# Performance work log

Hardware: AMD Instinct MI355X
Metric: run time of the kernel (lower is better)

## Reference

```python
import jax, jax.numpy as jnp
import numpy as np

H = 16  # n_heads


def _ln(x, g, b, eps=1e-5):
    m = x.mean(-1, keepdims=True)
    v = ((x - m) ** 2).mean(-1, keepdims=True)
    return (x - m) / jnp.sqrt(v + eps) * g + b


def setup_inputs() -> dict:
    key = jax.random.key(0)
    ks = jax.random.split(key, 10)
    b, lq, d, dff, L = 2, 1024, 1024, 4096, 4
    s = 0.02
    return {
        "x": jax.random.normal(ks[0], (b, lq, d), jnp.float32),
        "memory_bank": jax.random.normal(ks[1], (L, b, lq, d), jnp.float32),
        "attn_mask": jax.random.bernoulli(ks[2], 0.3, (b, lq, lq)),
        "ln1_g": jnp.ones((d,), jnp.float32),
        "ln1_b": jnp.zeros((d,), jnp.float32),
        "Wq": jax.random.normal(ks[3], (d, d), jnp.float32) * s,
        "Wk": jax.random.normal(ks[4], (d, d), jnp.float32) * s,
        "Wv": jax.random.normal(ks[5], (d, d), jnp.float32) * s,
        "Wo": jax.random.normal(ks[6], (d, d), jnp.float32) * s,
        "ln2_g": jnp.ones((d,), jnp.float32),
        "ln2_b": jnp.zeros((d,), jnp.float32),
        "W1": jax.random.normal(ks[7], (d, dff), jnp.float32) * s,
        "b1": jnp.zeros((dff,), jnp.float32),
        "W2": jax.random.normal(ks[8], (dff, d), jnp.float32) * s,
        "b2": jnp.zeros((d,), jnp.float32),
    }


def reference(x, memory_bank, attn_mask, ln1_g, ln1_b, Wq, Wk, Wv, Wo,
              ln2_g, ln2_b, W1, b1, W2, b2):
    # x: [b, lq, d]; memory_bank: [L, b, lk, d]; attn_mask: [b, lq, lk] bool (True = masked)
    b, lq, d = x.shape
    dh = d // H
    # preprocess_attn: LayerNorm (eval mode -> dropouts are identity)
    q = _ln(x, ln1_g, ln1_b)
    # grow memory bank with current normalized input
    mem = jnp.concatenate([memory_bank, q[None]], axis=0)  # [L+1, b, lk, d]
    L, _, lk, _ = mem.shape
    # projections (bias-free); key/value projected per layer then flattened over (L, lk)
    pq = (q @ Wq).reshape(b, lq, H, dh).transpose(0, 2, 1, 3) * (dh ** -0.5)  # [b,h,lq,dh]
    pk = (mem @ Wk).transpose(1, 0, 2, 3).reshape(b, L * lk, H, dh).transpose(0, 2, 1, 3)
    pv = (mem @ Wv).transpose(1, 0, 2, 3).reshape(b, L * lk, H, dh).transpose(0, 2, 1, 3)
    scores = jnp.einsum('bhqd,bhkd->bhqk', pq, pk)           # [b,h,lq,L*lk]
    scores = scores.reshape(b, H, lq, L, lk)
    scores = jnp.where(attn_mask[:, None, :, None, :], -jnp.inf, scores)
    attn = jax.nn.softmax(scores.reshape(b, H, lq, L * lk), axis=-1)
    ctx = jnp.einsum('bhqk,bhkd->bhqd', attn, pv)            # [b,h,lq,dh]
    ctx = ctx.transpose(0, 2, 1, 3).reshape(b, lq, d)
    attn_out = ctx @ Wo
    # postprocess_attn: residual add
    x2 = x + attn_out
    # FFN: LayerNorm -> Linear -> ReLU -> Linear -> residual
    f = _ln(x2, ln2_g, ln2_b)
    f = jax.nn.relu(f @ W1 + b1) @ W2 + b2
    out = x2 + f
    return (out, mem)
```

## Files before the change

### kernel.cpp

```cpp
#include <hip/hip_runtime.h>
#include <hip/hip_bf16.h>

typedef __attribute__((ext_vector_type(8))) __bf16 bf16x8;
typedef __attribute__((ext_vector_type(4))) __bf16 bf16x4;
typedef __attribute__((ext_vector_type(4))) float f32x4;
typedef __attribute__((ext_vector_type(16))) float f32x16;

#define MFMA16(a, b, c) __builtin_amdgcn_mfma_f32_16x16x32_bf16((a), (b), (c), 0, 0, 0)
#define MFMA32(a, b, c) __builtin_amdgcn_mfma_f32_32x32x16_bf16((a), (b), (c), 0, 0, 0)
#define LOG2E 1.4426950408889634f

static __device__ __forceinline__ float exp2_fast(float x) {
    float r; asm("v_exp_f32 %0, %1" : "=v"(r) : "v"(x)); return r;
}

__device__ __forceinline__ void gll16(const void* g, void* l) {
    __builtin_amdgcn_global_load_lds((const __attribute__((address_space(1))) void*)g,
                                     (__attribute__((address_space(3))) void*)l,
                                     16, 0, 0);
}

__global__ __launch_bounds__(256) void prep_kernel(const float* __restrict__ bank,
                                                   float* __restrict__ mem_out,
                                                   __bf16* __restrict__ membf,
                                                   const float* __restrict__ x,
                                                   const float* __restrict__ g,
                                                   const float* __restrict__ bta,
                                                   float* __restrict__ q_out,
                                                   __bf16* __restrict__ qbf,
                                                   const unsigned char* __restrict__ mask,
                                                   unsigned int* __restrict__ mbits) {
    __shared__ float rs[4], rs2[4];
    int blk = blockIdx.x;
    if (blk < 2048) {
        int i = blk * 256 + threadIdx.x;
        const float4* i4 = (const float4*)bank;
        float4* o4 = (float4*)mem_out;
        for (; i < 2097152; i += 2048 * 256) {
            float4 v = i4[i];
            o4[i] = v;
            if (membf) {
                bf16x4 ob = {(__bf16)v.x, (__bf16)v.y, (__bf16)v.z, (__bf16)v.w};
                ((bf16x4*)membf)[i] = ob;
            }
        }
    } else if (blk < 4096) {
        int row = blk - 2048;
        const float4 v = ((const float4*)(x + (size_t)row * 1024))[threadIdx.x];
        float s = v.x + v.y + v.z + v.w;
        float s2 = v.x * v.x + v.y * v.y + v.z * v.z + v.w * v.w;
#pragma unroll
        for (int off = 1; off < 64; off <<= 1) {
            s += __shfl_xor(s, off);
            s2 += __shfl_xor(s2, off);
        }
        int wv = threadIdx.x >> 6;
        if ((threadIdx.x & 63) == 0) { rs[wv] = s; rs2[wv] = s2; }
        __syncthreads();
        s = rs[0] + rs[1] + rs[2] + rs[3];
        s2 = rs2[0] + rs2[1] + rs2[2] + rs2[3];
        float mean = s * (1.0f / 1024.0f);
        float var = s2 * (1.0f / 1024.0f) - mean * mean;
        float rstd = rsqrtf(var + 1e-5f);
        float4 gg = ((const float4*)g)[threadIdx.x];
        float4 bb = ((const float4*)bta)[threadIdx.x];
        float4 o;
        o.x = (v.x - mean) * rstd * gg.x + bb.x;
        o.y = (v.y - mean) * rstd * gg.y + bb.y;
        o.z = (v.z - mean) * rstd * gg.z + bb.z;
        o.w = (v.w - mean) * rstd * gg.w + bb.w;
        ((float4*)(q_out + (size_t)row * 1024))[threadIdx.x] = o;
        if (qbf) {
            bf16x4 ob = {(__bf16)o.x, (__bf16)o.y, (__bf16)o.z, (__bf16)o.w};
            ((bf16x4*)(qbf + (size_t)row * 1024))[threadIdx.x] = ob;
        }
    } else if (mbits) {
        int row = blk - 4096;
        const unsigned char* mrow = mask + (size_t)row * 1024;
        int w = threadIdx.x >> 6, l = threadIdx.x & 63;
        unsigned long long* dst = (unsigned long long*)(mbits + (size_t)row * 32);
#pragma unroll
        for (int i = 0; i < 4; i++) {
            int key = i * 256 + w * 64 + l;
            unsigned long long bal = __ballot(mrow[key] != 0);
            if (l == 0) dst[i * 4 + w] = bal;
        }
    }
}

__global__ __launch_bounds__(256) void ln_kernel(const float* __restrict__ x,
                                                 const float* __restrict__ g,
                                                 const float* __restrict__ bta,
                                                 __bf16* __restrict__ outb) {
    int row = blockIdx.x;
    const float4 v = ((const float4*)(x + (size_t)row * 1024))[threadIdx.x];
    float s = v.x + v.y + v.z + v.w;
    float s2 = v.x * v.x + v.y * v.y + v.z * v.z + v.w * v.w;
#pragma unroll
    for (int off = 1; off < 64; off <<= 1) {
        s += __shfl_xor(s, off);
        s2 += __shfl_xor(s2, off);
    }
    __shared__ float rs[4], rs2[4];
    int wv = threadIdx.x >> 6;
    if ((threadIdx.x & 63) == 0) { rs[wv] = s; rs2[wv] = s2; }
    __syncthreads();
    s = rs[0] + rs[1] + rs[2] + rs[3];
    s2 = rs2[0] + rs2[1] + rs2[2] + rs2[3];
    float mean = s * (1.0f / 1024.0f);
    float var = s2 * (1.0f / 1024.0f) - mean * mean;
    float rstd = rsqrtf(var + 1e-5f);
    float4 gg = ((const float4*)g)[threadIdx.x];
    float4 bb = ((const float4*)bta)[threadIdx.x];
    bf16x4 ob;
    ob[0] = (__bf16)((v.x - mean) * rstd * gg.x + bb.x);
    ob[1] = (__bf16)((v.y - mean) * rstd * gg.y + bb.y);
    ob[2] = (__bf16)((v.z - mean) * rstd * gg.z + bb.z);
    ob[3] = (__bf16)((v.w - mean) * rstd * gg.w + bb.w);
    ((bf16x4*)(outb + (size_t)row * 1024))[threadIdx.x] = ob;
}

__global__ __launch_bounds__(256) void comb_ln2(const float* __restrict__ pc0,
                                                const float* __restrict__ pc1,
                                                const float* __restrict__ x,
                                                const float* __restrict__ g,
                                                const float* __restrict__ bta,
                                                float* __restrict__ x2,
                                                __bf16* __restrict__ fln) {
    int row = blockIdx.x;
    int idx = row * 256 + threadIdx.x;
    float4 a = ((const float4*)pc0)[idx];
    float4 b = ((const float4*)pc1)[idx];
    float4 r = ((const float4*)x)[idx];
    float4 v;
    v.x = a.x + b.x + r.x;
    v.y = a.y + b.y + r.y;
    v.z = a.z + b.z + r.z;
    v.w = a.w + b.w + r.w;
    ((float4*)x2)[idx] = v;
    float s = v.x + v.y + v.z + v.w;
    float s2 = v.x * v.x + v.y * v.y + v.z * v.z + v.w * v.w;
#pragma unroll
    for (int off = 1; off < 64; off <<= 1) {
        s += __shfl_xor(s, off);
        s2 += __shfl_xor(s2, off);
    }
    __shared__ float rs[4], rs2[4];
    int wv = threadIdx.x >> 6;
    if ((threadIdx.x & 63) == 0) { rs[wv] = s; rs2[wv] = s2; }
    __syncthreads();
    s = rs[0] + rs[1] + rs[2] + rs[3];
    s2 = rs2[0] + rs2[1] + rs2[2] + rs2[3];
    float mean = s * (1.0f / 1024.0f);
    float var = s2 * (1.0f / 1024.0f) - mean * mean;
    float rstd = rsqrtf(var + 1e-5f);
    float4 gg = ((const float4*)g)[threadIdx.x];
    float4 bb = ((const float4*)bta)[threadIdx.x];
    bf16x4 ob;
    ob[0] = (__bf16)((v.x - mean) * rstd * gg.x + bb.x);
    ob[1] = (__bf16)((v.y - mean) * rstd * gg.y + bb.y);
    ob[2] = (__bf16)((v.z - mean) * rstd * gg.z + bb.z);
    ob[3] = (__bf16)((v.w - mean) * rstd * gg.w + bb.w);
    ((bf16x4*)(fln + (size_t)row * 1024))[threadIdx.x] = ob;
}

__device__ __forceinline__ void tr_body(const float* __restrict__ in, __bf16* __restrict__ out,
                                        int K, int N, int k0, int n0) {
    __shared__ float tile[32][33];
    int tx = threadIdx.x & 31, ty = threadIdx.x >> 5;
#pragma unroll
    for (int i = 0; i < 4; i++)
        tile[ty + i * 8][tx] = in[(size_t)(k0 + ty + i * 8) * N + n0 + tx];
    __syncthreads();
#pragma unroll
    for (int i = 0; i < 4; i++)
        out[(size_t)(n0 + ty + i * 8) * K + k0 + tx] = (__bf16)tile[tx][ty + i * 8];
}

__global__ __launch_bounds__(256) void tr_early(const float* __restrict__ Wq,
                                                const float* __restrict__ Wk,
                                                const float* __restrict__ Wv,
                                                __bf16* __restrict__ Wq_t,
                                                __bf16* __restrict__ Wkv_t) {
    int w = blockIdx.x;
    int sel = w >> 10, within = w & 1023;
    const float* in = (sel == 0) ? Wq : ((sel == 1) ? Wk : Wv);
    __bf16* out = (sel == 0) ? Wq_t : (Wkv_t + (size_t)(sel - 1) * 1048576);
    tr_body(in, out, 1024, 1024, (within >> 5) * 32, (within & 31) * 32);
}

__global__ __launch_bounds__(256) void tr_late(const float* __restrict__ Wo,
                                               const float* __restrict__ W1,
                                               const float* __restrict__ W2,
                                               __bf16* __restrict__ Wo_t,
                                               __bf16* __restrict__ W1_t,
                                               __bf16* __restrict__ W2_t) {
    int w = blockIdx.x;
    const float* in;
    __bf16* out;
    int K, N, k0, n0;
    if (w < 1024) {
        in = Wo; out = Wo_t; K = 1024; N = 1024; n0 = (w & 31) * 32; k0 = (w >> 5) * 32;
    } else if (w < 5120) {
        int v = w - 1024;
        in = W1; out = W1_t; K = 1024; N = 4096; n0 = (v & 127) * 32; k0 = (v >> 7) * 32;
    } else {
        int v = w - 5120;
        in = W2; out = W2_t; K = 4096; N = 1024; n0 = (v & 31) * 32; k0 = (v >> 5) * 32;
    }
    tr_body(in, out, K, N, k0, n0);
}

template <int EPI, bool ABF16>
__device__ __forceinline__ void gemm_core(const void* __restrict__ Av,
                                          const __bf16* __restrict__ Bt,
                                          void* __restrict__ Cout,
                                          const float* __restrict__ bias,
                                          const float* __restrict__ res,
                                          int N, int lda, int ldb, int klen,
                                          float scale, int bm, int bn) {
    constexpr int LDA = ABF16 ? 32 : 40;
    __shared__ __bf16 As[128 * LDA];
    __shared__ __bf16 Bs[128 * 32];

    int t = threadIdx.x;
    int lane = t & 63, wave = t >> 6;
    int wm = (wave >> 1) * 64, wn = (wave & 1) * 64;
    int l16 = lane & 15, l4 = lane >> 4;

    f32x4 acc[4][4];
#pragma unroll
    for (int m = 0; m < 4; m++)
#pragma unroll
        for (int n = 0; n < 4; n++) acc[m][n] = (f32x4){0.f, 0.f, 0.f, 0.f};

    int srow = t >> 2;
    int scol = (t & 3) * 8;
    int ar = t >> 1, ak = (t & 1) * 16;
    const __bf16* Ab = (const __bf16*)Av;
    const float* Af = (const float*)Av;

    for (int k0 = 0; k0 < klen; k0 += 32) {
        gll16(Bt + (size_t)(bn + srow) * ldb + (k0 + scol), &Bs[wave * 512]);
        gll16(Bt + (size_t)(bn + 64 + srow) * ldb + (k0 + scol), &Bs[2048 + wave * 512]);
        if constexpr (ABF16) {
            gll16(Ab + (size_t)(bm + srow) * lda + (k0 + scol), &As[wave * 512]);
            gll16(Ab + (size_t)(bm + 64 + srow) * lda + (k0 + scol), &As[2048 + wave * 512]);
        } else {
            const float* ap = Af + (size_t)(bm + ar) * lda + k0 + ak;
            float4 f0 = ((const float4*)ap)[0];
            float4 f1 = ((const float4*)ap)[1];
            float4 f2 = ((const float4*)ap)[2];
            float4 f3 = ((const float4*)ap)[3];
            float ta[16] = {f0.x, f0.y, f0.z, f0.w, f1.x, f1.y, f1.z, f1.w,
                            f2.x, f2.y, f2.z, f2.w, f3.x, f3.y, f3.z, f3.w};
            bf16x8 v0, v1;
#pragma unroll
            for (int j = 0; j < 8; j++) { v0[j] = (__bf16)ta[j]; v1[j] = (__bf16)ta[j + 8]; }
            *(bf16x8*)&As[ar * 40 + ak] = v0;
            *(bf16x8*)&As[ar * 40 + ak + 8] = v1;
        }
        __syncthreads();

        bf16x8 af[4], bfr[4];
#pragma unroll
        for (int m = 0; m < 4; m++) af[m] = *(const bf16x8*)&As[(wm + m * 16 + l16) * LDA + l4 * 8];
#pragma unroll
        for (int n = 0; n < 4; n++) bfr[n] = *(const bf16x8*)&Bs[(wn + n * 16 + l16) * 32 + l4 * 8];
#pragma unroll
        for (int m = 0; m < 4; m++)
#pragma unroll
            for (int n = 0; n < 4; n++) acc[m][n] = MFMA16(af[m], bfr[n], acc[m][n]);
        __syncthreads();
    }

#pragma unroll
    for (int m = 0; m < 4; m++) {
#pragma unroll
        for (int r = 0; r < 4; r++) {
            int row = bm + wm + m * 16 + l4 * 4 + r;
#pragma unroll
            for (int n = 0; n < 4; n++) {
                int col = bn + wn + n * 16 + l16;
                float c = acc[m][n][r];
                size_t idx = (size_t)row * N + col;
                if (EPI == 0) {
                    ((__bf16*)Cout)[idx] = (__bf16)(c * scale);
                } else if (EPI == 1) {
                    ((float*)Cout)[idx] = c + res[idx];
                } else if (EPI == 2) {
                    ((__bf16*)Cout)[idx] = (__bf16)fmaxf(c + bias[col], 0.0f);
                } else if (EPI == 3) {
                    ((float*)Cout)[idx] = c + bias[col] + res[idx];
                } else {
                    ((float*)Cout)[idx] = c;
                }
            }
        }
    }
}

template <int EPI, bool ABF16>
__global__ __launch_bounds__(256) void gemm_bt(const void* __restrict__ Av,
                                               const __bf16* __restrict__ Bt,
                                               void* __restrict__ Cout,
                                               const float* __restrict__ bias,
                                               const float* __restrict__ res,
                                               int N, int K, float scale, int nbx) {
    int q = gridDim.x >> 3;
    int swz = (blockIdx.x & 7) * q + (blockIdx.x >> 3);
    int bn = (swz % nbx) * 128;
    int bm = (swz / nbx) * 128;
    gemm_core<EPI, ABF16>(Av, Bt, Cout, bias, res, N, K, K, K, scale, bm, bn);
}

template <bool ABF16>
__global__ __launch_bounds__(256) void gemm_proj(const void* __restrict__ Akv,
                                                 const __bf16* __restrict__ Wkv_t,
                                                 __bf16* __restrict__ PKV,
                                                 const void* __restrict__ Aq,
                                                 const __bf16* __restrict__ Wq_t,
                                                 __bf16* __restrict__ Pq) {
    int q = gridDim.x >> 3;
    int swz = (blockIdx.x & 7) * q + (blockIdx.x >> 3);
    const void* A;
    const __bf16* B;
    __bf16* C;
    int N, bm, bn;
    float sc;
    if (swz < 1280) {
        A = Akv; B = Wkv_t; C = PKV; N = 2048; sc = 1.0f;
        bn = (swz & 15) * 128; bm = (swz >> 4) * 128;
    } else {
        int p = swz - 1280;
        A = Aq; B = Wq_t; C = Pq; N = 1024; sc = 0.125f * LOG2E;
        bn = (p & 7) * 128; bm = (p >> 3) * 128;
    }
    gemm_core<0, ABF16>(A, B, C, nullptr, nullptr, N, 1024, 1024, 1024, sc, bm, bn);
}

__global__ __launch_bounds__(256) void gemm_w2(const __bf16* __restrict__ h1,
                                               const __bf16* __restrict__ W2_t,
                                               float* __restrict__ pc0,
                                               float* __restrict__ pc1) {
    int q = gridDim.x >> 3;
    int swz = (blockIdx.x & 7) * q + (blockIdx.x >> 3);
    int half = swz >> 7;
    int p = swz & 127;
    int bn = (p & 7) * 128, bm = (p >> 3) * 128;
    int koff = half * 2048;
    gemm_core<4, true>(h1 + koff, W2_t + koff, half ? pc1 : pc0, nullptr, nullptr,
                       1024, 4096, 4096, 2048, 1.0f, bm, bn);
}

__global__ __launch_bounds__(256) void gemm_wo(const __bf16* __restrict__ ctx,
                                               const __bf16* __restrict__ Wo_t,
                                               float* __restrict__ pc0,
                                               float* __restrict__ pc1) {
    int q = gridDim.x >> 3;
    int swz = (blockIdx.x & 7) * q + (blockIdx.x >> 3);
    int half = swz >> 7;
    int p = swz & 127;
    int bn = (p & 7) * 128, bm = (p >> 3) * 128;
    int koff = half * 512;
    gemm_core<4, true>(ctx + koff, Wo_t + koff, half ? pc1 : pc0, nullptr, nullptr,
                       1024, 1024, 1024, 512, 1.0f, bm, bn);
}

__global__ __launch_bounds__(256) void comb_kernel(const float* __restrict__ pc0,
                                                   const float* __restrict__ pc1,
                                                   const float* __restrict__ bias,
                                                   const float* __restrict__ res,
                                                   float* __restrict__ out) {
    int i = blockIdx.x * 256 + threadIdx.x;
    float4 a = ((const float4*)pc0)[i];
    float4 b = ((const float4*)pc1)[i];
    float4 r = ((const float4*)res)[i];
    float4 o;
    o.x = a.x + b.x + r.x;
    o.y = a.y + b.y + r.y;
    o.z = a.z + b.z + r.z;
    o.w = a.w + b.w + r.w;
    if (bias) {
        float4 bb = ((const float4*)bias)[i & 255];
        o.x += bb.x; o.y += bb.y; o.z += bb.z; o.w += bb.w;
    }
    ((float4*)out)[i] = o;
}

__device__ __forceinline__ void softmax_p(const f32x16& s0, const f32x16& s1,
                                          unsigned int mka, unsigned int mkb,
                                          int hi, float& lsum, bf16x8* pf) {
    unsigned int ow[8][2];
#pragma unroll
    for (int g = 0; g < 4; g++) {
        bf16x4 p0, p1;
#pragma unroll
        for (int m = 0; m < 4; m++) {
            float e = exp2_fast(s0[g * 4 + m]);
            e = ((mka >> (g * 8 + hi * 4 + m)) & 1u) ? 0.0f : e;
            lsum += e;
            p0[m] = (__bf16)e;
            float e2 = exp2_fast(s1[g * 4 + m]);
            e2 = ((mkb >> (g * 8 + hi * 4 + m)) & 1u) ? 0.0f : e2;
            lsum += e2;
            p1[m] = (__bf16)e2;
        }
        ow[g][0] = ((unsigned int*)&p0)[0];
        ow[g][1] = ((unsigned int*)&p0)[1];
        ow[4 + g][0] = ((unsigned int*)&p1)[0];
        ow[4 + g][1] = ((unsigned int*)&p1)[1];
    }
#pragma unroll
    for (int ks = 0; ks < 4; ks++) {
        unsigned int a0 = ow[2 * ks][0], b0 = ow[2 * ks + 1][0];
        unsigned int a1 = ow[2 * ks][1], b1 = ow[2 * ks + 1][1];
        asm volatile("v_permlane32_swap_b32 %0, %1" : "+v"(a0), "+v"(b0));
        asm volatile("v_permlane32_swap_b32 %0, %1" : "+v"(a1), "+v"(b1));
        unsigned int* pp = (unsigned int*)&pf[ks];
        pp[0] = a0; pp[1] = a1; pp[2] = b0; pp[3] = b1;
    }
}

#define NCHP 20
__global__ __launch_bounds__(256, 2) void attn_part(const __bf16* __restrict__ Pq,
                                                    const __bf16* __restrict__ PKV,
                                                    const unsigned int* __restrict__ mbits,
                                                    __bf16* __restrict__ pacc,
                                                    float* __restrict__ pl) {
    int bh = blockIdx.x;
    int b = bh >> 4, h = bh & 15;
    int rng = blockIdx.z;
    int wave = threadIdx.x >> 6, lane = threadIdx.x & 63;
    int l32 = lane & 31, hi = lane >> 5;
    int q0 = blockIdx.y * 256 + wave * 64;

    __shared__ __bf16 Ks[2][64][64];
    __shared__ __bf16 Vt[2][64][64];

    bf16x8 qf[2][4];
#pragma unroll
    for (int tile = 0; tile < 2; tile++) {
        const __bf16* pqrow = Pq + (size_t)(b * 1024 + q0 + tile * 32 + l32) * 1024 + h * 64 + hi * 8;
#pragma unroll
        for (int ds = 0; ds < 4; ds++) qf[tile][ds] = *(const bf16x8*)(pqrow + ds * 16);
    }

    f32x16 acc00, acc01, acc10, acc11;
#pragma unroll
    for (int i = 0; i < 16; i++) { acc00[i] = 0.f; acc01[i] = 0.f; acc10[i] = 0.f; acc11[i] = 0.f; }
    float lsum0 = 0.0f, lsum1 = 0.0f;

    const unsigned int* mrow0 = mbits + (size_t)(b * 1024 + q0 + l32) * 32;
    const unsigned int* mrow1 = mbits + (size_t)(b * 1024 + q0 + 32 + l32) * 32;

    int tl = threadIdx.x;
    int skey = tl >> 2, sd0 = (tl & 3) << 4;
    int kgbase = rng * 1280;

    int Gk = (skey ^ (skey >> 3)) & 7;
    int kw0 = skey * 64 + ((((sd0 >> 3) + 0) ^ Gk) << 3);
    int kw1 = skey * 64 + ((((sd0 >> 3) + 1) ^ Gk) << 3);
    int vwa[16];
#pragma unroll
    for (int j = 0; j < 16; j++) {
        int row = sd0 + j;
        int Gr = (row ^ (row >> 3)) & 7;
        vwa[j] = row * 64 + ((((skey >> 3) ^ Gr) << 3) | (skey & 7));
    }
    __bf16* KsF = &Ks[0][0][0];
    __bf16* VtF = &Vt[0][0][0];

    int Gr0 = (l32 ^ (l32 >> 3)) & 7;
    int r1v = 32 + l32;
    int Gr1 = (r1v ^ (r1v >> 3)) & 7;

    bf16x8 rk0, rk1, rv0, rv1;

    {
        int kg = kgbase + skey;
        int lidx = kg >> 10, i = kg & 1023;
        size_t off = ((size_t)(lidx * 2048 + b * 1024 + i) << 11) + h * 64 + sd0;
        rk0 = *(const bf16x8*)(PKV + off);
        rk1 = *(const bf16x8*)(PKV + off + 8);
        rv0 = *(const bf16x8*)(PKV + off + 1024);
        rv1 = *(const bf16x8*)(PKV + off + 1032);
    }
    *(bf16x8*)&KsF[kw0] = rk0;
    *(bf16x8*)&KsF[kw1] = rk1;
#pragma unroll
    for (int j = 0; j < 8; j++) { VtF[vwa[j]] = rv0[j]; VtF[vwa[j + 8]] = rv1[j]; }
    {
        int kg = kgbase + 64 + skey;
        int lidx = kg >> 10, i = kg & 1023;
        size_t off = ((size_t)(lidx * 2048 + b * 1024 + i) << 11) + h * 64 + sd0;
        rk0 = *(const bf16x8*)(PKV + off);
        rk1 = *(const bf16x8*)(PKV + off + 8);
        rv0 = *(const bf16x8*)(PKV + off + 1024);
        rv1 = *(const bf16x8*)(PKV + off + 1032);
    }
    int kd0 = (kgbase & 1023) >> 5;
    unsigned int mk0a = mrow0[kd0], mk0b = mrow0[kd0 + 1];
    unsigned int mk1a = mrow1[kd0], mk1b = mrow1[kd0 + 1];

    for (int t = 0; t < NCHP; t++) {
        int cbo = (t & 1) << 12;
        int nbo = cbo ^ 4096;
        __syncthreads();
        if (t + 1 < NCHP) {
            *(bf16x8*)&KsF[nbo + kw0] = rk0;
            *(bf16x8*)&KsF[nbo + kw1] = rk1;
#pragma unroll
            for (int j = 0; j < 8; j++) { VtF[nbo + vwa[j]] = rv0[j]; VtF[nbo + vwa[j + 8]] = rv1[j]; }
        }
        if (t + 2 < NCHP) {
            int kg = kgbase + (t + 2) * 64 + skey;
            int lidx = kg >> 10, i = kg & 1023;
            size_t off = ((size_t)(lidx * 2048 + b * 1024 + i) << 11) + h * 64 + sd0;
            rk0 = *(const bf16x8*)(PKV + off);
            rk1 = *(const bf16x8*)(PKV + off + 8);
            rv0 = *(const bf16x8*)(PKV + off + 1024);
            rv1 = *(const bf16x8*)(PKV + off + 1032);
        }
        unsigned int nk0a = 0, nk0b = 0, nk1a = 0, nk1b = 0;
        if (t + 1 < NCHP) {
            int kdn = ((kgbase + (t + 1) * 64) & 1023) >> 5;
            nk0a = mrow0[kdn]; nk0b = mrow0[kdn + 1];
            nk1a = mrow1[kdn]; nk1b = mrow1[kdn + 1];
        }

        f32x16 s00, s01, s10, s11;
#pragma unroll
        for (int i = 0; i < 16; i++) { s00[i] = 0.f; s01[i] = 0.f; s10[i] = 0.f; s11[i] = 0.f; }
        __builtin_amdgcn_s_setprio(1);
#pragma unroll
        for (int ds = 0; ds < 4; ds++) {
            bf16x8 ka0 = *(const bf16x8*)&KsF[cbo + l32 * 64 + (((ds * 2 + hi) ^ Gr0) << 3)];
            bf16x8 ka1 = *(const bf16x8*)&KsF[cbo + r1v * 64 + (((ds * 2 + hi) ^ Gr1) << 3)];
            s00 = MFMA32(ka0, qf[0][ds], s00);
            s10 = MFMA32(ka0, qf[1][ds], s10);
            s01 = MFMA32(ka1, qf[0][ds], s01);
            s11 = MFMA32(ka1, qf[1][ds], s11);
        }
        __builtin_amdgcn_s_setprio(0);

        bf16x8 pf0[4], pf1[4];
        softmax_p(s00, s01, mk0a, mk0b, hi, lsum0, pf0);
        softmax_p(s10, s11, mk1a, mk1b, hi, lsum1, pf1);

        mk0a = nk0a; mk0b = nk0b; mk1a = nk1a; mk1b = nk1b;

        __builtin_amdgcn_s_setprio(1);
#pragma unroll
        for (int ks = 0; ks < 4; ks++) {
            bf16x8 vf0 = *(const bf16x8*)&VtF[cbo + l32 * 64 + (((ks * 2 + hi) ^ Gr0) << 3)];
            bf16x8 vf1 = *(const bf16x8*)&VtF[cbo + r1v * 64 + (((ks * 2 + hi) ^ Gr1) << 3)];
            acc00 = MFMA32(vf0, pf0[ks], acc00);
            acc01 = MFMA32(vf1, pf0[ks], acc01);
            acc10 = MFMA32(vf0, pf1[ks], acc10);
            acc11 = MFMA32(vf1, pf1[ks], acc11);
        }
        __builtin_amdgcn_s_setprio(0);
    }

    lsum0 += __shfl_xor(lsum0, 32);
    lsum1 += __shfl_xor(lsum1, 32);

    size_t blk = ((size_t)(bh * 4 + blockIdx.y) * 4 + rng);
    __bf16* pa0 = pacc + blk * 16384 + (size_t)(wave * 64 + l32) * 64;
    __bf16* pa1 = pacc + blk * 16384 + (size_t)(wave * 64 + 32 + l32) * 64;
#pragma unroll
    for (int g = 0; g < 4; g++) {
        bf16x4 o00, o01, o10, o11;
#pragma unroll
        for (int m = 0; m < 4; m++) {
            o00[m] = (__bf16)acc00[g * 4 + m];
            o01[m] = (__bf16)acc01[g * 4 + m];
            o10[m] = (__bf16)acc10[g * 4 + m];
            o11[m] = (__bf16)acc11[g * 4 + m];
        }
        *(bf16x4*)&pa0[g * 8 + hi * 4] = o00;
        *(bf16x4*)&pa0[32 + g * 8 + hi * 4] = o01;
        *(bf16x4*)&pa1[g * 8 + hi * 4] = o10;
        *(bf16x4*)&pa1[32 + g * 8 + hi * 4] = o11;
    }
    if (hi == 0) {
        pl[blk * 256 + wave * 64 + l32] = lsum0;
        pl[blk * 256 + wave * 64 + 32 + l32] = lsum1;
    }
}

__global__ __launch_bounds__(512) void attn_comb(const __bf16* __restrict__ pacc,
                                                 const float* __restrict__ pl,
                                                 __bf16* __restrict__ ctx) {
    int bh = blockIdx.x, qb = blockIdx.y;
    int b = bh >> 4, h = bh & 15;
    int q = threadIdx.x >> 1, dhalf = (threadIdx.x & 1) * 32;
    float acc[32];
#pragma unroll
    for (int j = 0; j < 32; j++) acc[j] = 0.0f;
    float l = 0.0f;
    size_t blk0 = ((size_t)(bh * 4 + qb)) * 4;
#pragma unroll
    for (int rng = 0; rng < 4; rng++) {
        size_t base = (blk0 + rng) * 16384 + (size_t)q * 64 + dhalf;
#pragma unroll
        for (int v = 0; v < 4; v++) {
            bf16x8 a = *(const bf16x8*)&pacc[base + v * 8];
#pragma unroll
            for (int j = 0; j < 8; j++) acc[v * 8 + j] += (float)a[j];
        }
        l += pl[(blk0 + rng) * 256 + q];
    }
    float inv = 1.0f / l;
    __bf16* crow = ctx + ((size_t)(b * 1024 + qb * 256 + q) << 10) + h * 64 + dhalf;
#pragma unroll
    for (int v = 0; v < 4; v++) {
        bf16x8 o;
#pragma unroll
        for (int j = 0; j < 8; j++) o[j] = (__bf16)(acc[v * 8 + j] * inv);
        *(bf16x8*)&crow[v * 8] = o;
    }
}

#define KHALF 2560
#define CK 64
#define NCH 40
__global__ __launch_bounds__(512, 4) void attn_kernel(const __bf16* __restrict__ Pq,
                                                      const __bf16* __restrict__ PKV,
                                                      const unsigned char* __restrict__ mask,
                                                      __bf16* __restrict__ ctx) {
    int bh = blockIdx.x;
    int b = bh >> 4, h = bh & 15;
    int wave = threadIdx.x >> 6, lane = threadIdx.x & 63;
    int grp = wave >> 2, wv = wave & 3;
    int l16 = lane & 15, l4 = lane >> 4;
    int q0 = blockIdx.y * 64 + wv * 16;

    __shared__ __bf16 Ks[2][64][72];
    __shared__ __bf16 Vt[2][64][72];
    __shared__ __bf16 Ps[8][16][72];

    const f32x4 fzero = {0.f, 0.f, 0.f, 0.f};

    bf16x8 qf[2];
    {
        const __bf16* pqrow = Pq + (size_t)(b * 1024 + q0 + l16) * 1024 + h * 64;
        qf[0] = *(const bf16x8*)(pqrow + l4 * 8);
        qf[1] = *(const bf16x8*)(pqrow + 32 + l4 * 8);
    }

    f32x4 accT[4];
#pragma unroll
    for (int n = 0; n < 4; n++) accT[n] = fzero;
    float lsum = 0.0f;

    const unsigned char* mrow_p = mask + (size_t)b * (1024u * 1024u) + (size_t)(q0 + l16) * 1024;

    int tl = threadIdx.x & 255;
    int skey = tl >> 2;
    int sd0 = (tl & 3) << 4;
    int kgbase = grp * KHALF;

    bf16x8 rk0, rk1, rv0, rv1;
    unsigned int mk[4], mkn[4];
    {
        int kg = kgbase + skey;
        int lidx = kg >> 10, i = kg & 1023;
        size_t off = ((size_t)(lidx * 2048 + b * 1024 + i) << 11) + h * 64 + sd0;
        rk0 = *(const bf16x8*)(PKV + off);
        rk1 = *(const bf16x8*)(PKV + off + 8);
        rv0 = *(const bf16x8*)(PKV + off + 1024);
        rv1 = *(const bf16x8*)(PKV + off + 1032);
        int kloc = kgbase & 1023;
#pragma unroll
        for (int tile = 0; tile < 4; tile++)
            mk[tile] = *(const unsigned int*)(mrow_p + kloc + tile * 16 + l4 * 4);
    }

    for (int t = 0; t < NCH; t++) {
        *(bf16x8*)&Ks[grp][skey][sd0] = rk0;
        *(bf16x8*)&Ks[grp][skey][sd0 + 8] = rk1;
#pragma unroll
        for (int j = 0; j < 8; j++) {
            int row = sd0 + j;
            Vt[grp][row][skey ^ ((row >> 3) << 3)] = rv0[j];
            int row2 = sd0 + 8 + j;
            Vt[grp][row2][skey ^ ((row2 >> 3) << 3)] = rv1[j];
        }
        __syncthreads();

        if (t + 1 < NCH) {
            int kg = kgbase + (t + 1) * CK + skey;
            int lidx = kg >> 10, i = kg & 1023;
            size_t off = ((size_t)(lidx * 2048 + b * 1024 + i) << 11) + h * 64 + sd0;
            rk0 = *(const bf16x8*)(PKV + off);
            rk1 = *(const bf16x8*)(PKV + off + 8);
            rv0 = *(const bf16x8*)(PKV + off + 1024);
            rv1 = *(const bf16x8*)(PKV + off + 1032);
            int kloc = (kgbase + (t + 1) * CK) & 1023;
#pragma unroll
            for (int tile = 0; tile < 4; tile++)
                mkn[tile] = *(const unsigned int*)(mrow_p + kloc + tile * 16 + l4 * 4);
        }

        f32x4 s[4];
        __builtin_amdgcn_s_setprio(1);
#pragma unroll
        for (int tile = 0; tile < 4; tile++) {
            bf16x8 ka = *(const bf16x8*)&Ks[grp][tile * 16 + l16][l4 * 8];
            bf16x8 kb = *(const bf16x8*)&Ks[grp][tile * 16 + l16][32 + l4 * 8];
            f32x4 sz = fzero;
            sz = MFMA16(ka, qf[0], sz);
            sz = MFMA16(kb, qf[1], sz);
            s[tile] = sz;
        }
        __builtin_amdgcn_s_setprio(0);

        float psum = 0.0f;
#pragma unroll
        for (int tile = 0; tile < 4; tile++) {
            bf16x4 pk_;
#pragma unroll
            for (int r = 0; r < 4; r++) {
                float e = exp2_fast(s[tile][r]);
                e = ((mk[tile] >> (r * 8)) & 255u) ? 0.0f : e;
                psum += e;
                pk_[r] = (__bf16)e;
            }
            *(bf16x4*)&Ps[wave][l16][tile * 16 + l4 * 4] = pk_;
        }
        lsum += psum;
#pragma unroll
        for (int tile = 0; tile < 4; tile++) mk[tile] = mkn[tile];

        __builtin_amdgcn_s_setprio(1);
#pragma unroll
        for (int kk = 0; kk < 2; kk++) {
            bf16x8 pf = *(const bf16x8*)&Ps[wave][l16][kk * 32 + l4 * 8];
#pragma unroll
            for (int n = 0; n < 4; n++) {
                int row = n * 16 + l16;
                int colblk = (kk * 32 + l4 * 8) ^ ((row >> 3) << 3);
                bf16x8 vf = *(const bf16x8*)&Vt[grp][row][colblk];
                accT[n] = MFMA16(vf, pf, accT[n]);
            }
        }
        __builtin_amdgcn_s_setprio(0);
        __syncthreads();
    }

    lsum += __shfl_xor(lsum, 16);
    lsum += __shfl_xor(lsum, 32);

    float* exAcc = (float*)&Ks[0][0][0];
    float* exL = (float*)&Vt[0][0][0];
    if (grp == 1) {
#pragma unroll
        for (int n = 0; n < 4; n++)
            *(f32x4*)&exAcc[(wv * 16 + l16) * 68 + n * 16 + l4 * 4] = accT[n];
        if (l4 == 0) exL[wv * 16 + l16] = lsum;
    }
    __syncthreads();
    if (grp == 0) {
        int qi = wv * 16 + l16;
        float inv = 1.0f / (lsum + exL[qi]);
        __bf16* crow = ctx + ((size_t)(b * 1024 + q0 + l16) << 10) + h * 64;
#pragma unroll
        for (int n = 0; n < 4; n++) {
            f32x4 a1 = *(const f32x4*)&exAcc[qi * 68 + n * 16 + l4 * 4];
            bf16x4 o;
#pragma unroll
            for (int r = 0; r < 4; r++) o[r] = (__bf16)((accT[n][r] + a1[r]) * inv);
            *(bf16x4*)&crow[n * 16 + l4 * 4] = o;
        }
    }
}

extern "C" void kernel_launch(void* const* d_in, const int* in_sizes, int n_in,
                              void* d_out, int out_size, void* d_ws, size_t ws_size,
                              hipStream_t stream) {
    const float* x = (const float*)d_in[0];
    const float* memory_bank = (const float*)d_in[1];
    const unsigned char* attn_mask = (const unsigned char*)d_in[2];
    const float* ln1_g = (const float*)d_in[3];
    const float* ln1_b = (const float*)d_in[4];
    const float* Wq = (const float*)d_in[5];
    const float* Wk = (const float*)d_in[6];
    const float* Wv = (const float*)d_in[7];
    const float* Wo = (const float*)d_in[8];
    const float* ln2_g = (const float*)d_in[9];
    const float* ln2_b = (const float*)d_in[10];
    const float* W1 = (const float*)d_in[11];
    const float* b1 = (const float*)d_in[12];
    const float* W2 = (const float*)d_in[13];
    const float* b2 = (const float*)d_in[14];

    float* out = (float*)d_out;
    float* mem_out = out + 2097152;
    float* q_out = mem_out + 4 * 2097152;

    char* ws = (char*)d_ws;
    bool big = ws_size >= (70ull << 20);

    __bf16* PKV = (__bf16*)ws;
    __bf16 *Pq, *Wq_t, *Wkv_t, *ctx, *membf = nullptr, *qbf = nullptr;
    __bf16* pacc = nullptr;
    float* plv = nullptr;
    unsigned int* mbits = nullptr;
    if (big) {
        membf = (__bf16*)(ws + (40ull << 20));
        qbf = membf + (size_t)8192 * 1024;
        Wq_t = (__bf16*)(ws + (60ull << 20));
        Wkv_t = (__bf16*)(ws + (62ull << 20));
        Pq = (__bf16*)(ws + (66ull << 20));
        ctx = (__bf16*)(ws + (60ull << 20));
        pacc = (__bf16*)(ws + (40ull << 20));
        plv = (float*)(ws + (56ull << 20));
        mbits = (unsigned int*)(ws + (30ull << 20));
    } else {
        Pq = (__bf16*)(ws + (40ull << 20));
        Wq_t = (__bf16*)(ws + (44ull << 20));
        Wkv_t = (__bf16*)(ws + (46ull << 20));
        ctx = (__bf16*)(ws + (44ull << 20));
    }
    __bf16* Wo_t = (__bf16*)ws;
    __bf16* W1_t = (__bf16*)(ws + (2ull << 20));
    __bf16* W2_t = (__bf16*)(ws + (10ull << 20));
    float* x2 = (float*)(ws + (18ull << 20));
    __bf16* fln = (__bf16*)(ws + (26ull << 20));
    __bf16* h1 = (__bf16*)(ws + (30ull << 20));
    float* wo_pc0 = (float*)(ws + (30ull << 20));
    float* wo_pc1 = (float*)(ws + (38ull << 20));
    float* pc0 = (float*)(ws + (46ull << 20));
    float* pc1 = (float*)(ws + (54ull << 20));

    prep_kernel<<<6144, 256, 0, stream>>>(memory_bank, mem_out, membf, x, ln1_g, ln1_b,
                                          q_out, qbf, attn_mask, mbits);
    tr_early<<<3072, 256, 0, stream>>>(Wq, Wk, Wv, Wq_t, Wkv_t);

    if (big)
        gemm_proj<true><<<1408, 256, 0, stream>>>(membf, Wkv_t, PKV, qbf, Wq_t, Pq);
    else
        gemm_proj<false><<<1408, 256, 0, stream>>>(mem_out, Wkv_t, PKV, q_out, Wq_t, Pq);

    if (big) {
        attn_part<<<dim3(32, 4, 4), 256, 0, stream>>>(Pq, PKV, mbits, pacc, plv);
        attn_comb<<<dim3(32, 4), 512, 0, stream>>>(pacc, plv, ctx);
    } else {
        attn_kernel<<<dim3(32, 16), 512, 0, stream>>>(Pq, PKV, attn_mask, ctx);
    }

    tr_late<<<9216, 256, 0, stream>>>(Wo, W1, W2, Wo_t, W1_t, W2_t);

    if (big) {
        gemm_wo<<<256, 256, 0, stream>>>(ctx, Wo_t, wo_pc0, wo_pc1);
        comb_ln2<<<2048, 256, 0, stream>>>(wo_pc0, wo_pc1, x, ln2_g, ln2_b, x2, fln);
    } else {
        gemm_bt<1, true><<<128, 256, 0, stream>>>(ctx, Wo_t, x2, nullptr, x, 1024, 1024, 1.0f, 8);
        ln_kernel<<<2048, 256, 0, stream>>>(x2, ln2_g, ln2_b, fln);
    }
    gemm_bt<2, true><<<512, 256, 0, stream>>>(fln, W1_t, h1, b1, nullptr, 4096, 1024, 1.0f, 32);
    if (big) {
        gemm_w2<<<256, 256, 0, stream>>>(h1, W2_t, pc0, pc1);
        comb_kernel<<<2048, 256, 0, stream>>>(pc0, pc1, b2, x2, out);
    } else {
        gemm_bt<3, true><<<128, 256, 0, stream>>>(h1, W2_t, out, b2, x2, 1024, 4096, 1.0f, 8);
    }
}
```

Baseline: 271.7 us.

## Pre-transpose V and stage K/V via async global-to-LDS loads in attention

```diff
diff --git a/kernel.cpp b/kernel.cpp
--- a/kernel.cpp
+++ b/kernel.cpp
@@ -28,9 +28,13 @@
                                                    const float* __restrict__ bta,
                                                    float* __restrict__ q_out,
                                                    __bf16* __restrict__ qbf,
-                                                   const unsigned char* __restrict__ mask,
-                                                   unsigned int* __restrict__ mbits) {
+                                                   const float* __restrict__ Wq,
+                                                   const float* __restrict__ Wk,
+                                                   const float* __restrict__ Wv,
+                                                   __bf16* __restrict__ Wq_t,
+                                                   __bf16* __restrict__ Wkv_t) {
     __shared__ float rs[4], rs2[4];
+    __shared__ float tile[32][33];
     int blk = blockIdx.x;
     if (blk < 2048) {
         int i = blk * 256 + threadIdx.x;
@@ -74,16 +78,59 @@
             bf16x4 ob = {(__bf16)o.x, (__bf16)o.y, (__bf16)o.z, (__bf16)o.w};
             ((bf16x4*)(qbf + (size_t)row * 1024))[threadIdx.x] = ob;
         }
-    } else if (mbits) {
-        int row = blk - 4096;
+    } else {
+        int w = blk - 4096;
+        int sel = w >> 10, within = w & 1023;
+        const float* in = (sel == 0) ? Wq : ((sel == 1) ? Wk : Wv);
+        __bf16* out = (sel == 0) ? Wq_t : (Wkv_t + (size_t)(sel - 1) * 1048576);
+        int k0 = (within >> 5) * 32, n0 = (within & 31) * 32;
+        int tx = threadIdx.x & 31, ty = threadIdx.x >> 5;
+#pragma unroll
+        for (int i = 0; i < 4; i++)
+            tile[ty + i * 8][tx] = in[(size_t)(k0 + ty + i * 8) * 1024 + n0 + tx];
+        __syncthreads();
+#pragma unroll
+        for (int i = 0; i < 4; i++)
+            out[(size_t)(n0 + ty + i * 8) * 1024 + k0 + tx] = (__bf16)tile[tx][ty + i * 8];
+    }
+}
+
+__global__ __launch_bounds__(256) void vtr_kernel(const __bf16* __restrict__ PV,
+                                                  __bf16* __restrict__ PVt,
+                                                  const unsigned char* __restrict__ mask,
+                                                  unsigned int* __restrict__ mbits) {
+    __shared__ __bf16 tile[64][72];
+    int w = blockIdx.x;
+    if (w < 2560) {
+        int bh = w / 80, kt = w % 80;
+        int b = bh >> 4, h = bh & 15;
+        int lidx = kt >> 4, i0 = (kt & 15) * 64;
+        int kg0 = lidx * 2048 + b * 1024 + i0;
+        int r = threadIdx.x >> 2, c16 = (threadIdx.x & 3) * 16;
+        const __bf16* src = PV + (size_t)(kg0 + r) * 1024 + h * 64 + c16;
+        *(bf16x8*)&tile[r][c16] = *(const bf16x8*)src;
+        *(bf16x8*)&tile[r][c16 + 8] = *(const bf16x8*)(src + 8);
+        __syncthreads();
+        int dh = threadIdx.x >> 2, k0 = (threadIdx.x & 3) * 16;
+        bf16x8 o0, o1;
+#pragma unroll
+        for (int j = 0; j < 8; j++) {
+            o0[j] = tile[k0 + j][dh];
+            o1[j] = tile[k0 + 8 + j][dh];
+        }
+        __bf16* dst = PVt + (size_t)(bh * 64 + dh) * 5120 + kt * 64 + k0;
+        *(bf16x8*)dst = o0;
+        *(bf16x8*)(dst + 8) = o1;
+    } else {
+        int row = w - 2560;
         const unsigned char* mrow = mask + (size_t)row * 1024;
-        int w = threadIdx.x >> 6, l = threadIdx.x & 63;
+        int wv = threadIdx.x >> 6, l = threadIdx.x & 63;
         unsigned long long* dst = (unsigned long long*)(mbits + (size_t)row * 32);
 #pragma unroll
         for (int i = 0; i < 4; i++) {
-            int key = i * 256 + w * 64 + l;
+            int key = i * 256 + wv * 64 + l;
             unsigned long long bal = __ballot(mrow[key] != 0);
-            if (l == 0) dst[i * 4 + w] = bal;
+            if (l == 0) dst[i * 4 + wv] = bal;
         }
     }
 }
@@ -177,18 +224,6 @@
         out[(size_t)(n0 + ty + i * 8) * K + k0 + tx] = (__bf16)tile[tx][ty + i * 8];
 }
 
-__global__ __launch_bounds__(256) void tr_early(const float* __restrict__ Wq,
-                                                const float* __restrict__ Wk,
-                                                const float* __restrict__ Wv,
-                                                __bf16* __restrict__ Wq_t,
-                                                __bf16* __restrict__ Wkv_t) {
-    int w = blockIdx.x;
-    int sel = w >> 10, within = w & 1023;
-    const float* in = (sel == 0) ? Wq : ((sel == 1) ? Wk : Wv);
-    __bf16* out = (sel == 0) ? Wq_t : (Wkv_t + (size_t)(sel - 1) * 1048576);
-    tr_body(in, out, 1024, 1024, (within >> 5) * 32, (within & 31) * 32);
-}
-
 __global__ __launch_bounds__(256) void tr_late(const float* __restrict__ Wo,
                                                const float* __restrict__ W1,
                                                const float* __restrict__ W2,
@@ -317,26 +352,25 @@
 template <bool ABF16>
 __global__ __launch_bounds__(256) void gemm_proj(const void* __restrict__ Akv,
                                                  const __bf16* __restrict__ Wkv_t,
-                                                 __bf16* __restrict__ PKV,
+                                                 __bf16* __restrict__ PK,
+                                                 __bf16* __restrict__ PV,
                                                  const void* __restrict__ Aq,
                                                  const __bf16* __restrict__ Wq_t,
                                                  __bf16* __restrict__ Pq) {
     int q = gridDim.x >> 3;
     int swz = (blockIdx.x & 7) * q + (blockIdx.x >> 3);
-    const void* A;
-    const __bf16* B;
-    __bf16* C;
-    int N, bm, bn;
-    float sc;
     if (swz < 1280) {
-        A = Akv; B = Wkv_t; C = PKV; N = 2048; sc = 1.0f;
-        bn = (swz & 15) * 128; bm = (swz >> 4) * 128;
+        int bn = (swz & 15) * 128, bm = (swz >> 4) * 128;
+        __bf16* C = (bn < 1024) ? PK : PV;
+        int bnl = bn & 1023;
+        const __bf16* Bt = Wkv_t + ((size_t)(bn & 1024) << 10);
+        gemm_core<0, ABF16>(Akv, Bt, C, nullptr, nullptr, 1024, 1024, 1024, 1024, 1.0f, bm, bnl);
     } else {
         int p = swz - 1280;
-        A = Aq; B = Wq_t; C = Pq; N = 1024; sc = 0.125f * LOG2E;
-        bn = (p & 7) * 128; bm = (p >> 3) * 128;
-    }
-    gemm_core<0, ABF16>(A, B, C, nullptr, nullptr, N, 1024, 1024, 1024, sc, bm, bn);
+        int bn = (p & 7) * 128, bm = (p >> 3) * 128;
+        gemm_core<0, ABF16>(Aq, Wq_t, Pq, nullptr, nullptr, 1024, 1024, 1024, 1024,
+                            0.125f * LOG2E, bm, bn);
+    }
 }
 
 __global__ __launch_bounds__(256) void gemm_w2(const __bf16* __restrict__ h1,
@@ -424,7 +458,8 @@
 
 #define NCHP 20
 __global__ __launch_bounds__(256, 2) void attn_part(const __bf16* __restrict__ Pq,
-                                                    const __bf16* __restrict__ PKV,
+                                                    const __bf16* __restrict__ PK,
+                                                    const __bf16* __restrict__ PVt,
                                                     const unsigned int* __restrict__ mbits,
                                                     __bf16* __restrict__ pacc,
                                                     float* __restrict__ pl) {
@@ -435,8 +470,8 @@
     int l32 = lane & 31, hi = lane >> 5;
     int q0 = blockIdx.y * 256 + wave * 64;
 
-    __shared__ __bf16 Ks[2][64][64];
-    __shared__ __bf16 Vt[2][64][64];
+    __shared__ __bf16 KB[2][64][64];
+    __shared__ __bf16 VB[2][64][64];
 
     bf16x8 qf[2][4];
 #pragma unroll
@@ -454,73 +489,55 @@
     const unsigned int* mrow0 = mbits + (size_t)(b * 1024 + q0 + l32) * 32;
     const unsigned int* mrow1 = mbits + (size_t)(b * 1024 + q0 + 32 + l32) * 32;
 
-    int tl = threadIdx.x;
-    int skey = tl >> 2, sd0 = (tl & 3) << 4;
     int kgbase = rng * 1280;
 
-    int Gk = (skey ^ (skey >> 3)) & 7;
-    int kw0 = skey * 64 + ((((sd0 >> 3) + 0) ^ Gk) << 3);
-    int kw1 = skey * 64 + ((((sd0 >> 3) + 1) ^ Gk) << 3);
-    int vwa[16];
-#pragma unroll
-    for (int j = 0; j < 16; j++) {
-        int row = sd0 + j;
-        int Gr = (row ^ (row >> 3)) & 7;
-        vwa[j] = row * 64 + ((((skey >> 3) ^ Gr) << 3) | (skey & 7));
-    }
-    __bf16* KsF = &Ks[0][0][0];
-    __bf16* VtF = &Vt[0][0][0];
+    int idxA = wave * 8 + (lane >> 3);
+    int idxB = (wave + 4) * 8 + (lane >> 3);
+    int GA = (idxA ^ (idxA >> 3)) & 7;
+    int GB = (idxB ^ (idxB >> 3)) & 7;
+    int swA = (((lane & 7) ^ GA) << 4);
+    int swB = (((lane & 7) ^ GB) << 4);
+    size_t koffA = (size_t)idxA * 2048 + swA;
+    size_t koffB = (size_t)idxB * 2048 + swB;
+    size_t voffA = (size_t)idxA * 10240 + swA;
+    size_t voffB = (size_t)idxB * 10240 + swB;
+
+    int kmod = kgbase & 1023;
+    const char* pkc = (const char*)PK + ((size_t)((kgbase >> 10) * 2048 + b * 1024 + kmod)) * 2048
+                      + (size_t)h * 128;
+    const char* pvc = (const char*)PVt + (size_t)(bh * 64) * 10240 + (size_t)kgbase * 2;
+
+#define STAGE(BUF)                                            \
+    do {                                                      \
+        gll16(pkc + koffA, &KB[BUF][wave * 8][0]);            \
+        gll16(pkc + koffB, &KB[BUF][(wave + 4) * 8][0]);      \
+        gll16(pvc + voffA, &VB[BUF][wave * 8][0]);            \
+        gll16(pvc + voffB, &VB[BUF][(wave + 4) * 8][0]);      \
+    } while (0)
+#define ADV()                                                          \
+    do {                                                               \
+        int st = (kmod + 64 >= 1024) ? (64 + 1024) : 64;               \
+        kmod = (kmod + 64) & 1023;                                     \
+        pkc += (size_t)st * 2048;                                      \
+        pvc += 128;                                                    \
+    } while (0)
+
+    STAGE(0);
+    ADV();
+    int kd0 = (kgbase & 1023) >> 5;
+    unsigned int mk0a = mrow0[kd0], mk0b = mrow0[kd0 + 1];
+    unsigned int mk1a = mrow1[kd0], mk1b = mrow1[kd0 + 1];
 
     int Gr0 = (l32 ^ (l32 >> 3)) & 7;
     int r1v = 32 + l32;
     int Gr1 = (r1v ^ (r1v >> 3)) & 7;
 
-    bf16x8 rk0, rk1, rv0, rv1;
-
-    {
-        int kg = kgbase + skey;
-        int lidx = kg >> 10, i = kg & 1023;
-        size_t off = ((size_t)(lidx * 2048 + b * 1024 + i) << 11) + h * 64 + sd0;
-        rk0 = *(const bf16x8*)(PKV + off);
-        rk1 = *(const bf16x8*)(PKV + off + 8);
-        rv0 = *(const bf16x8*)(PKV + off + 1024);
-        rv1 = *(const bf16x8*)(PKV + off + 1032);
-    }
-    *(bf16x8*)&KsF[kw0] = rk0;
-    *(bf16x8*)&KsF[kw1] = rk1;
-#pragma unroll
-    for (int j = 0; j < 8; j++) { VtF[vwa[j]] = rv0[j]; VtF[vwa[j + 8]] = rv1[j]; }
-    {
-        int kg = kgbase + 64 + skey;
-        int lidx = kg >> 10, i = kg & 1023;
-        size_t off = ((size_t)(lidx * 2048 + b * 1024 + i) << 11) + h * 64 + sd0;
-        rk0 = *(const bf16x8*)(PKV + off);
-        rk1 = *(const bf16x8*)(PKV + off + 8);
-        rv0 = *(const bf16x8*)(PKV + off + 1024);
-        rv1 = *(const bf16x8*)(PKV + off + 1032);
-    }
-    int kd0 = (kgbase & 1023) >> 5;
-    unsigned int mk0a = mrow0[kd0], mk0b = mrow0[kd0 + 1];
-    unsigned int mk1a = mrow1[kd0], mk1b = mrow1[kd0 + 1];
-
     for (int t = 0; t < NCHP; t++) {
-        int cbo = (t & 1) << 12;
-        int nbo = cbo ^ 4096;
+        int buf = t & 1;
         __syncthreads();
         if (t + 1 < NCHP) {
-            *(bf16x8*)&KsF[nbo + kw0] = rk0;
-            *(bf16x8*)&KsF[nbo + kw1] = rk1;
-#pragma unroll
-            for (int j = 0; j < 8; j++) { VtF[nbo + vwa[j]] = rv0[j]; VtF[nbo + vwa[j + 8]] = rv1[j]; }
-        }
-        if (t + 2 < NCHP) {
-            int kg = kgbase + (t + 2) * 64 + skey;
-            int lidx = kg >> 10, i = kg & 1023;
-            size_t off = ((size_t)(lidx * 2048 + b * 1024 + i) << 11) + h * 64 + sd0;
-            rk0 = *(const bf16x8*)(PKV + off);
-            rk1 = *(const bf16x8*)(PKV + off + 8);
-            rv0 = *(const bf16x8*)(PKV + off + 1024);
-            rv1 = *(const bf16x8*)(PKV + off + 1032);
+            STAGE(buf ^ 1);
+            ADV();
         }
         unsigned int nk0a = 0, nk0b = 0, nk1a = 0, nk1b = 0;
         if (t + 1 < NCHP) {
@@ -529,14 +546,17 @@
             nk1a = mrow1[kdn]; nk1b = mrow1[kdn + 1];
         }
 
+        const __bf16* KsF = &KB[buf][0][0];
+        const __bf16* VtF = &VB[buf][0][0];
+
         f32x16 s00, s01, s10, s11;
 #pragma unroll
         for (int i = 0; i < 16; i++) { s00[i] = 0.f; s01[i] = 0.f; s10[i] = 0.f; s11[i] = 0.f; }
         __builtin_amdgcn_s_setprio(1);
 #pragma unroll
         for (int ds = 0; ds < 4; ds++) {
-            bf16x8 ka0 = *(const bf16x8*)&KsF[cbo + l32 * 64 + (((ds * 2 + hi) ^ Gr0) << 3)];
-            bf16x8 ka1 = *(const bf16x8*)&KsF[cbo + r1v * 64 + (((ds * 2 + hi) ^ Gr1) << 3)];
+            bf16x8 ka0 = *(const bf16x8*)&KsF[l32 * 64 + (((ds * 2 + hi) ^ Gr0) << 3)];
+            bf16x8 ka1 = *(const bf16x8*)&KsF[r1v * 64 + (((ds * 2 + hi) ^ Gr1) << 3)];
             s00 = MFMA32(ka0, qf[0][ds], s00);
             s10 = MFMA32(ka0, qf[1][ds], s10);
             s01 = MFMA32(ka1, qf[0][ds], s01);
@@ -553,8 +573,8 @@
         __builtin_amdgcn_s_setprio(1);
 #pragma unroll
         for (int ks = 0; ks < 4; ks++) {
-            bf16x8 vf0 = *(const bf16x8*)&VtF[cbo + l32 * 64 + (((ks * 2 + hi) ^ Gr0) << 3)];
-            bf16x8 vf1 = *(const bf16x8*)&VtF[cbo + r1v * 64 + (((ks * 2 + hi) ^ Gr1) << 3)];
+            bf16x8 vf0 = *(const bf16x8*)&VtF[l32 * 64 + (((ks * 2 + hi) ^ Gr0) << 3)];
+            bf16x8 vf1 = *(const bf16x8*)&VtF[r1v * 64 + (((ks * 2 + hi) ^ Gr1) << 3)];
             acc00 = MFMA32(vf0, pf0[ks], acc00);
             acc01 = MFMA32(vf1, pf0[ks], acc01);
             acc10 = MFMA32(vf0, pf1[ks], acc10);
@@ -562,6 +582,8 @@
         }
         __builtin_amdgcn_s_setprio(0);
     }
+#undef STAGE
+#undef ADV
 
     lsum0 += __shfl_xor(lsum0, 32);
     lsum1 += __shfl_xor(lsum1, 32);
@@ -627,7 +649,8 @@
 #define CK 64
 #define NCH 40
 __global__ __launch_bounds__(512, 4) void attn_kernel(const __bf16* __restrict__ Pq,
-                                                      const __bf16* __restrict__ PKV,
+                                                      const __bf16* __restrict__ PK,
+                                                      const __bf16* __restrict__ PV,
                                                       const unsigned char* __restrict__ mask,
                                                       __bf16* __restrict__ ctx) {
     int bh = blockIdx.x;
@@ -667,11 +690,11 @@
     {
         int kg = kgbase + skey;
         int lidx = kg >> 10, i = kg & 1023;
-        size_t off = ((size_t)(lidx * 2048 + b * 1024 + i) << 11) + h * 64 + sd0;
-        rk0 = *(const bf16x8*)(PKV + off);
-        rk1 = *(const bf16x8*)(PKV + off + 8);
-        rv0 = *(const bf16x8*)(PKV + off + 1024);
-        rv1 = *(const bf16x8*)(PKV + off + 1032);
+        size_t off = (size_t)(lidx * 2048 + b * 1024 + i) * 1024 + h * 64 + sd0;
+        rk0 = *(const bf16x8*)(PK + off);
+        rk1 = *(const bf16x8*)(PK + off + 8);
+        rv0 = *(const bf16x8*)(PV + off);
+        rv1 = *(const bf16x8*)(PV + off + 8);
         int kloc = kgbase & 1023;
 #pragma unroll
         for (int tile = 0; tile < 4; tile++)
@@ -693,11 +716,11 @@
         if (t + 1 < NCH) {
             int kg = kgbase + (t + 1) * CK + skey;
             int lidx = kg >> 10, i = kg & 1023;
-            size_t off = ((size_t)(lidx * 2048 + b * 1024 + i) << 11) + h * 64 + sd0;
-            rk0 = *(const bf16x8*)(PKV + off);
-            rk1 = *(const bf16x8*)(PKV + off + 8);
-            rv0 = *(const bf16x8*)(PKV + off + 1024);
-            rv1 = *(const bf16x8*)(PKV + off + 1032);
+            size_t off = (size_t)(lidx * 2048 + b * 1024 + i) * 1024 + h * 64 + sd0;
+            rk0 = *(const bf16x8*)(PK + off);
+            rk1 = *(const bf16x8*)(PK + off + 8);
+            rv0 = *(const bf16x8*)(PV + off);
+            rv1 = *(const bf16x8*)(PV + off + 8);
             int kloc = (kgbase + (t + 1) * CK) & 1023;
 #pragma unroll
             for (int tile = 0; tile < 4; tile++)
@@ -803,8 +826,10 @@
     char* ws = (char*)d_ws;
     bool big = ws_size >= (70ull << 20);
 
-    __bf16* PKV = (__bf16*)ws;
+    __bf16* PK = (__bf16*)ws;
+    __bf16* PV = (__bf16*)(ws + (20ull << 20));
     __bf16 *Pq, *Wq_t, *Wkv_t, *ctx, *membf = nullptr, *qbf = nullptr;
+    __bf16* PVt = nullptr;
     __bf16* pacc = nullptr;
     float* plv = nullptr;
     unsigned int* mbits = nullptr;
@@ -814,10 +839,11 @@
         Wq_t = (__bf16*)(ws + (60ull << 20));
         Wkv_t = (__bf16*)(ws + (62ull << 20));
         Pq = (__bf16*)(ws + (66ull << 20));
+        PVt = (__bf16*)(ws + (40ull << 20));
+        mbits = (unsigned int*)(ws + (60ull << 20));
+        pacc = (__bf16*)(ws + (20ull << 20));
+        plv = (float*)(ws + (36ull << 20));
         ctx = (__bf16*)(ws + (60ull << 20));
-        pacc = (__bf16*)(ws + (40ull << 20));
-        plv = (float*)(ws + (56ull << 20));
-        mbits = (unsigned int*)(ws + (30ull << 20));
     } else {
         Pq = (__bf16*)(ws + (40ull << 20));
         Wq_t = (__bf16*)(ws + (44ull << 20));
@@ -835,20 +861,20 @@
     float* pc0 = (float*)(ws + (46ull << 20));
     float* pc1 = (float*)(ws + (54ull << 20));
 
-    prep_kernel<<<6144, 256, 0, stream>>>(memory_bank, mem_out, membf, x, ln1_g, ln1_b,
-                                          q_out, qbf, attn_mask, mbits);
-    tr_early<<<3072, 256, 0, stream>>>(Wq, Wk, Wv, Wq_t, Wkv_t);
+    prep_kernel<<<7168, 256, 0, stream>>>(memory_bank, mem_out, membf, x, ln1_g, ln1_b,
+                                          q_out, qbf, Wq, Wk, Wv, Wq_t, Wkv_t);
 
     if (big)
-        gemm_proj<true><<<1408, 256, 0, stream>>>(membf, Wkv_t, PKV, qbf, Wq_t, Pq);
+        gemm_proj<true><<<1408, 256, 0, stream>>>(membf, Wkv_t, PK, PV, qbf, Wq_t, Pq);
     else
-        gemm_proj<false><<<1408, 256, 0, stream>>>(mem_out, Wkv_t, PKV, q_out, Wq_t, Pq);
+        gemm_proj<false><<<1408, 256, 0, stream>>>(mem_out, Wkv_t, PK, PV, q_out, Wq_t, Pq);
 
     if (big) {
-        attn_part<<<dim3(32, 4, 4), 256, 0, stream>>>(Pq, PKV, mbits, pacc, plv);
+        vtr_kernel<<<4608, 256, 0, stream>>>(PV, PVt, attn_mask, mbits);
+        attn_part<<<dim3(32, 4, 4), 256, 0, stream>>>(Pq, PK, PVt, mbits, pacc, plv);
         attn_comb<<<dim3(32, 4), 512, 0, stream>>>(pacc, plv, ctx);
     } else {
-        attn_kernel<<<dim3(32, 16), 512, 0, stream>>>(Pq, PKV, attn_mask, ctx);
+        attn_kernel<<<dim3(32, 16), 512, 0, stream>>>(Pq, PK, PV, attn_mask, ctx);
     }
 
     tr_late<<<9216, 256, 0, stream>>>(Wo, W1, W2, Wo_t, W1_t, W2_t);
```

New measurement: 272.9 us. Within noise of the previous version (+0.4%).
